# Performance work log

Measured on AMD Instinct MI355X. Metric: run time of the kernel, lower is better.

The kernel has to match this reference:

```python
import jax, jax.numpy as jnp
import numpy as np

B, S, D, H = 4, 2048, 1024, 16
HD = D // H  # head dim = 64


def setup_inputs() -> dict:
    key = jax.random.key(0)
    ks = jax.random.split(key, 11)
    std = 1.0 / np.sqrt(D)
    return {
        "query": jax.random.normal(ks[0], (B, S, D), jnp.float32),
        "key": jax.random.normal(ks[1], (B, S, D), jnp.float32),
        "value": jax.random.normal(ks[2], (B, S, D), jnp.float32),
        "Wq": jax.random.normal(ks[3], (D, D), jnp.float32) * std,
        "bq": jnp.zeros((D,), jnp.float32),
        "Wk": jax.random.normal(ks[4], (D, D), jnp.float32) * std,
        "bk": jnp.zeros((D,), jnp.float32),
        "Wv": jax.random.normal(ks[5], (D, D), jnp.float32) * std,
        "bv": jnp.zeros((D,), jnp.float32),
        "Wo": jax.random.normal(ks[6], (D, D), jnp.float32) * std,
        "bo": jnp.zeros((D,), jnp.float32),
    }


def reference(query, key, value, Wq, bq, Wk, bk, Wv, bv, Wo, bo):
    scale = jnp.sqrt(jnp.float32(D))  # NOTE: module scales by sqrt(hid_dim), not sqrt(head_dim)
    # nn.Linear: x @ W.T + b
    def split_heads(x):
        return x.reshape(B, -1, H, HD).transpose(0, 2, 1, 3)  # [B,H,S,HD]
    Q = split_heads(query @ Wq.T + bq)
    K = split_heads(key @ Wk.T + bk)
    V = split_heads(value @ Wv.T + bv)
    energy = jnp.einsum("bhqd,bhkd->bhqk", Q, K) / scale  # [B,H,S,S]
    attention = jax.nn.softmax(energy, axis=-1)  # dropout is identity in eval / p=0
    X = jnp.einsum("bhqk,bhkd->bhqd", attention, V)  # [B,H,S,HD]
    X = X.transpose(0, 2, 1, 3).reshape(B, -1, D)  # [B,S,D]
    return X @ Wo.T + bo
```

## Files before the change

### kernel.cpp

```cpp
#include <hip/hip_runtime.h>
#include <stdint.h>

#define DEVI __device__ __forceinline__

typedef __attribute__((ext_vector_type(8))) __bf16 bf16x8;
typedef __attribute__((ext_vector_type(4))) __bf16 bf16x4;
typedef __attribute__((ext_vector_type(4))) float f32x4;
typedef __attribute__((ext_vector_type(4))) unsigned short u16x4;
typedef __attribute__((ext_vector_type(4))) unsigned int u32x4;
typedef unsigned short u16;

constexpr int Bn = 4, Sn = 2048, Dn = 1024, Hn = 16;
constexpr int Mn = Bn * Sn;
constexpr float QSCALE = 1.4426950408889634f / 32.0f;
constexpr float SSHIFT = -16.0f;

DEVI u16 f2bf(float f) {
  uint32_t u = __builtin_bit_cast(uint32_t, f);
  u += 0x7fffu + ((u >> 16) & 1u);
  return (u16)(u >> 16);
}

typedef __attribute__((address_space(1))) void gvoid;
typedef __attribute__((address_space(3))) void lvoid;
DEVI void gload_lds16(const void* g, void* l) {
  __builtin_amdgcn_global_load_lds((gvoid*)(uintptr_t)g,
                                   (lvoid*)(uint32_t)(uintptr_t)l, 16, 0, 0);
}

DEVI f32x4 mfma16(bf16x8 a, bf16x8 b, f32x4 c) {
  return __builtin_amdgcn_mfma_f32_16x16x32_bf16(a, b, c, 0, 0, 0);
}

struct CastArgs {
  const float* src[7];
  u16* dst[7];
  int n[7];
};

__global__ __launch_bounds__(256) void cast_kernel(CastArgs a) {
  const int seg = blockIdx.y;
  const float* __restrict__ src = a.src[seg];
  u16* __restrict__ dst = a.dst[seg];
  const int n = a.n[seg];
  const int stride = gridDim.x * 256 * 4;
  for (int i = (blockIdx.x * 256 + threadIdx.x) * 4; i < n; i += stride) {
    const float4 v = *reinterpret_cast<const float4*>(src + i);
    u16x4 p;
    p[0] = f2bf(v.x); p[1] = f2bf(v.y); p[2] = f2bf(v.z); p[3] = f2bf(v.w);
    *reinterpret_cast<u16x4*>(dst + i) = p;
  }
}

struct QKVArgs {
  const u16 *Aq, *Ak, *Av, *Wq, *Wk, *Wv;
  const float *bq, *bk, *bv;
  u16 *Qh, *Kh, *Vt;
};

__global__ __launch_bounds__(256)
void qkv_gemm(QKVArgs a) {
  constexpr int BK = 32, Kd = 1024;
  __shared__ __align__(16) u16 As[128 * BK];
  __shared__ __align__(16) u16 Bs[128 * BK];

  const int raw = blockIdx.x;
  const int swz = (raw & 7) * 192 + (raw >> 3);
  const int which = swz >> 9;
  const int bid = swz & 511;
  const u16* __restrict__ A  = which == 0 ? a.Aq : which == 1 ? a.Ak : a.Av;
  const u16* __restrict__ Bt = which == 0 ? a.Wq : which == 1 ? a.Wk : a.Wv;
  const float* __restrict__ bias = which == 0 ? a.bq : which == 1 ? a.bk : a.bv;

  const int tid = threadIdx.x;
  const int lane = tid & 63;
  const int w = tid >> 6;
  const int wr = w >> 1, wc = w & 1;
  const int mt = bid >> 3, nt = bid & 7;
  const int m0 = mt * 128, n0 = nt * 128;
  const int c = lane & 15, g = lane >> 4;

  f32x4 acc[4][4] = {};

  const u16* aA[2];
  const u16* aB[2];
  int loff[2];
  #pragma unroll
  for (int i = 0; i < 2; ++i) {
    const int chunk = (i * 4 + w) * 64 + lane;
    const int row = chunk >> 2, col = (chunk & 3) * 8;
    aA[i] = A + (size_t)(m0 + row) * Kd + col;
    aB[i] = Bt + (size_t)(n0 + row) * Kd + col;
    loff[i] = (i * 4 + w) * 1024;
  }

  for (int kt = 0; kt < Kd; kt += BK) {
    #pragma unroll
    for (int i = 0; i < 2; ++i) {
      gload_lds16(aA[i] + kt, (char*)As + loff[i]);
      gload_lds16(aB[i] + kt, (char*)Bs + loff[i]);
    }
    __syncthreads();
    bf16x8 af[4], bfr[4];
    #pragma unroll
    for (int i = 0; i < 4; ++i) {
      af[i]  = *(const bf16x8*)(As + (wr * 64 + i * 16 + c) * BK + g * 8);
      bfr[i] = *(const bf16x8*)(Bs + (wc * 64 + i * 16 + c) * BK + g * 8);
    }
    #pragma unroll
    for (int mi = 0; mi < 4; ++mi)
      #pragma unroll
      for (int ni = 0; ni < 4; ++ni)
        acc[mi][ni] = mfma16(af[mi], bfr[ni], acc[mi][ni]);
    __syncthreads();
  }

  #pragma unroll
  for (int mi = 0; mi < 4; ++mi) {
    #pragma unroll
    for (int ni = 0; ni < 4; ++ni) {
      const int n = n0 + wc * 64 + ni * 16 + c;
      const float bv = bias[n];
      const int mb = m0 + wr * 64 + mi * 16 + g * 4;
      const f32x4 v = acc[mi][ni];
      const int h = n >> 6, hd = n & 63;
      if (which == 2) {
        const int b = mb >> 11, s = mb & 2047;
        u16x4 pk;
        #pragma unroll
        for (int j = 0; j < 4; ++j) pk[j] = f2bf(v[j] + bv);
        *(u16x4*)(a.Vt + ((size_t)((b * Hn + h) * 64 + hd)) * Sn + s) = pk;
      } else {
        u16* dst = which == 0 ? a.Qh : a.Kh;
        const float sc = which == 0 ? QSCALE : 1.0f;
        #pragma unroll
        for (int j = 0; j < 4; ++j) {
          const int m = mb + j;
          const int b = m >> 11, s = m & 2047;
          dst[(((size_t)(b * Hn + h) * Sn + s) << 6) + hd] = f2bf((v[j] + bv) * sc);
        }
      }
    }
  }
}

__global__ __launch_bounds__(256)
void gemm_out(const u16* __restrict__ A, const u16* __restrict__ Bt,
              const float* __restrict__ bias, float* __restrict__ out) {
  constexpr int BK = 32, Kd = 1024;
  __shared__ __align__(16) u16 As[128 * BK];
  __shared__ __align__(16) u16 Bs[128 * BK];

  const int raw = blockIdx.x;
  const int swz = (raw & 7) * 64 + (raw >> 3);
  const int tid = threadIdx.x;
  const int lane = tid & 63;
  const int w = tid >> 6;
  const int wr = w >> 1, wc = w & 1;
  const int mt = swz >> 3, nt = swz & 7;
  const int m0 = mt * 128, n0 = nt * 128;
  const int c = lane & 15, g = lane >> 4;

  f32x4 acc[4][4] = {};

  const u16* aA[2];
  const u16* aB[2];
  int loff[2];
  #pragma unroll
  for (int i = 0; i < 2; ++i) {
    const int chunk = (i * 4 + w) * 64 + lane;
    const int row = chunk >> 2, col = (chunk & 3) * 8;
    aA[i] = A + (size_t)(m0 + row) * Kd + col;
    aB[i] = Bt + (size_t)(n0 + row) * Kd + col;
    loff[i] = (i * 4 + w) * 1024;
  }

  for (int kt = 0; kt < Kd; kt += BK) {
    #pragma unroll
    for (int i = 0; i < 2; ++i) {
      gload_lds16(aA[i] + kt, (char*)As + loff[i]);
      gload_lds16(aB[i] + kt, (char*)Bs + loff[i]);
    }
    __syncthreads();
    bf16x8 af[4], bfr[4];
    #pragma unroll
    for (int i = 0; i < 4; ++i) {
      af[i]  = *(const bf16x8*)(As + (wr * 64 + i * 16 + c) * BK + g * 8);
      bfr[i] = *(const bf16x8*)(Bs + (wc * 64 + i * 16 + c) * BK + g * 8);
    }
    #pragma unroll
    for (int mi = 0; mi < 4; ++mi)
      #pragma unroll
      for (int ni = 0; ni < 4; ++ni)
        acc[mi][ni] = mfma16(af[mi], bfr[ni], acc[mi][ni]);
    __syncthreads();
  }

  #pragma unroll
  for (int mi = 0; mi < 4; ++mi) {
    #pragma unroll
    for (int ni = 0; ni < 4; ++ni) {
      const int n = n0 + wc * 64 + ni * 16 + c;
      const float bv = bias[n];
      const int mb = m0 + wr * 64 + mi * 16 + g * 4;
      const f32x4 v = acc[mi][ni];
      #pragma unroll
      for (int j = 0; j < 4; ++j)
        out[(size_t)(mb + j) * Dn + n] = v[j] + bv;
    }
  }
}

__global__ __launch_bounds__(512, 4)
void flash_attn(const u16* __restrict__ Q, const u16* __restrict__ K,
                const u16* __restrict__ Vt, u16* __restrict__ X) {
  __shared__ __align__(16) u16 Ks[3][4096];
  __shared__ __align__(16) u16 Vs[3][4096];

  const int tid = threadIdx.x, lane = tid & 63, w = tid >> 6;
  const int bid = blockIdx.x;
  const int bh = bid & 63, qt = bid >> 6;
  const int b = bh >> 4, h = bh & 15;
  const int q0 = qt * 128 + w * 16;
  const int c = lane & 15, g = lane >> 4;

  const u16* Qb = Q + (size_t)bh * Sn * 64;
  const u16* Kb = K + (size_t)bh * Sn * 64;
  const u16* Vb = Vt + (size_t)bh * 64 * Sn;

  const int srow = tid >> 3;
  const int scol = (((tid & 7) * 16) ^ ((srow & 7) << 4)) >> 1;
  const int srcK = srow * 64 + scol;
  const int srcV = srow * Sn + scol;
  const int ldsOff = w * 1024;
#define STAGE(BUF, KV_)                                                   \
  {                                                                       \
    gload_lds16(Kb + (size_t)(KV_) * 64 + srcK, (char*)Ks[BUF] + ldsOff); \
    gload_lds16(Vb + (KV_) + srcV, (char*)Vs[BUF] + ldsOff);              \
  }

  const int laneB0 = c * 128 + ((g * 16) ^ ((c & 7) << 4));
  const int laneB1 = c * 128 + ((64 + g * 16) ^ ((c & 7) << 4));

  bf16x8 qf[2];
  #pragma unroll
  for (int ks = 0; ks < 2; ++ks)
    qf[ks] = *(const bf16x8*)(Qb + (size_t)(q0 + c) * 64 + ks * 32 + g * 8);

  bf16x8 ONES;
  #pragma unroll
  for (int e = 0; e < 8; ++e) ONES[e] = (__bf16)1.0f;
  const f32x4 SINITv = {SSHIFT, SSHIFT, SSHIFT, SSHIFT};

  STAGE(0, 0);
  STAGE(1, 64);

  f32x4 o[4] = {};
  f32x4 lacc = {};

#define TILE(BUF, SBUF, KV)                                                   \
  {                                                                           \
    asm volatile("s_waitcnt vmcnt(2)" ::: "memory");                          \
    __builtin_amdgcn_sched_barrier(0);                                        \
    __builtin_amdgcn_s_barrier();                                             \
    __builtin_amdgcn_sched_barrier(0);                                        \
    STAGE(SBUF, ((KV) + 128) & (Sn - 1));                                     \
    f32x4 sc[4];                                                              \
    {                                                                         \
      bf16x8 kfr[4];                                                          \
      _Pragma("unroll")                                                       \
      for (int kf = 0; kf < 4; ++kf)                                          \
        kfr[kf] = *(const bf16x8*)((const char*)Ks[BUF] + laneB0 + kf * 2048);\
      __builtin_amdgcn_s_setprio(1);                                          \
      _Pragma("unroll")                                                       \
      for (int kf = 0; kf < 4; ++kf)                                          \
        sc[kf] = mfma16(kfr[kf], qf[0], SINITv);                              \
      __builtin_amdgcn_s_setprio(0);                                          \
      _Pragma("unroll")                                                       \
      for (int kf = 0; kf < 4; ++kf)                                          \
        kfr[kf] = *(const bf16x8*)((const char*)Ks[BUF] + laneB1 + kf * 2048);\
      __builtin_amdgcn_s_setprio(1);                                          \
      _Pragma("unroll")                                                       \
      for (int kf = 0; kf < 4; ++kf)                                          \
        sc[kf] = mfma16(kfr[kf], qf[1], sc[kf]);                              \
      __builtin_amdgcn_s_setprio(0);                                          \
    }                                                                         \
    uint32_t wvv[4][2];                                                       \
    _Pragma("unroll")                                                         \
    for (int kf = 0; kf < 4; ++kf) {                                          \
      const float p0 = __builtin_exp2f(sc[kf][0]);                            \
      const float p1 = __builtin_exp2f(sc[kf][1]);                            \
      const float p2 = __builtin_exp2f(sc[kf][2]);                            \
      const float p3 = __builtin_exp2f(sc[kf][3]);                            \
      asm("v_cvt_pk_bf16_f32 %0, %1, %2" : "=v"(wvv[kf][0]) : "v"(p0), "v"(p1)); \
      asm("v_cvt_pk_bf16_f32 %0, %1, %2" : "=v"(wvv[kf][1]) : "v"(p2), "v"(p3)); \
    }                                                                         \
    bf16x8 pa[2];                                                             \
    _Pragma("unroll")                                                         \
    for (int ks2 = 0; ks2 < 2; ++ks2) {                                       \
      uint32_t ua = wvv[2 * ks2][0], ub = wvv[2 * ks2][1];                    \
      uint32_t uc = wvv[2 * ks2 + 1][0], ud = wvv[2 * ks2 + 1][1];            \
      asm("v_permlane32_swap_b32 %0, %1" : "+v"(ua), "+v"(uc));               \
      asm("v_permlane32_swap_b32 %0, %1" : "+v"(ub), "+v"(ud));               \
      asm("v_permlane16_swap_b32 %0, %1" : "+v"(ua), "+v"(uc));               \
      asm("v_permlane16_swap_b32 %0, %1" : "+v"(ub), "+v"(ud));               \
      const u32x4 uv = {ua, ub, uc, ud};                                      \
      pa[ks2] = __builtin_bit_cast(bf16x8, uv);                               \
    }                                                                         \
    lacc = mfma16(pa[0], ONES, lacc);                                         \
    lacc = mfma16(pa[1], ONES, lacc);                                         \
    {                                                                         \
      bf16x8 vfr[4];                                                          \
      _Pragma("unroll")                                                       \
      for (int nd = 0; nd < 4; ++nd)                                          \
        vfr[nd] = *(const bf16x8*)((const char*)Vs[BUF] + laneB0 + nd * 2048);\
      __builtin_amdgcn_s_setprio(1);                                          \
      _Pragma("unroll")                                                       \
      for (int nd = 0; nd < 4; ++nd)                                          \
        o[nd] = mfma16(pa[0], vfr[nd], o[nd]);                                \
      __builtin_amdgcn_s_setprio(0);                                          \
      _Pragma("unroll")                                                       \
      for (int nd = 0; nd < 4; ++nd)                                          \
        vfr[nd] = *(const bf16x8*)((const char*)Vs[BUF] + laneB1 + nd * 2048);\
      __builtin_amdgcn_s_setprio(1);                                          \
      _Pragma("unroll")                                                       \
      for (int nd = 0; nd < 4; ++nd)                                          \
        o[nd] = mfma16(pa[1], vfr[nd], o[nd]);                                \
      __builtin_amdgcn_s_setprio(0);                                          \
    }                                                                         \
  }

  for (int kv = 0; kv < 1920; kv += 192) {
    TILE(0, 2, kv);
    TILE(1, 0, kv + 64);
    TILE(2, 1, kv + 128);
  }
  TILE(0, 2, 1920);
  TILE(1, 0, 1984);
#undef TILE
#undef STAGE

  #pragma unroll
  for (int j = 0; j < 4; ++j) {
    const float rn = 1.0f / lacc[j];
    const int s = q0 + g * 4 + j;
    u16* dst = X + (size_t)(b * Sn + s) * Dn + h * 64 + c;
    #pragma unroll
    for (int nd = 0; nd < 4; ++nd)
      dst[nd * 16] = f2bf(o[nd][j] * rn);
  }
}

extern "C" void kernel_launch(void* const* d_in, const int* in_sizes, int n_in,
                              void* d_out, int out_size, void* d_ws, size_t ws_size,
                              hipStream_t stream) {
  (void)in_sizes; (void)n_in; (void)out_size; (void)ws_size;
  const float* query = (const float*)d_in[0];
  const float* key_  = (const float*)d_in[1];
  const float* value = (const float*)d_in[2];
  const float* Wq = (const float*)d_in[3];
  const float* bq = (const float*)d_in[4];
  const float* Wk = (const float*)d_in[5];
  const float* bk = (const float*)d_in[6];
  const float* Wv = (const float*)d_in[7];
  const float* bv = (const float*)d_in[8];
  const float* Wo = (const float*)d_in[9];
  const float* bo = (const float*)d_in[10];

  char* ws = (char*)d_ws;
  size_t off = 0;
  auto alloc = [&](size_t bytes) {
    void* p = ws + off;
    off += (bytes + 255) & ~(size_t)255;
    return p;
  };
  const size_t actB = (size_t)Mn * Dn * 2;
  const size_t wB = (size_t)Dn * Dn * 2;
  u16* qbuf = (u16*)alloc(actB);
  u16* kbuf = (u16*)alloc(actB);
  u16* vbuf = (u16*)alloc(actB);
  u16* wqb = (u16*)alloc(wB);
  u16* wkb = (u16*)alloc(wB);
  u16* wvb = (u16*)alloc(wB);
  u16* wob = (u16*)alloc(wB);
  u16* Qh = (u16*)alloc(actB);
  u16* Kh = (u16*)alloc(actB);
  u16* Vt = (u16*)alloc(actB);
  u16* Xb = qbuf;

  CastArgs ca;
  ca.src[0] = query; ca.src[1] = key_; ca.src[2] = value;
  ca.src[3] = Wq; ca.src[4] = Wk; ca.src[5] = Wv; ca.src[6] = Wo;
  ca.dst[0] = qbuf; ca.dst[1] = kbuf; ca.dst[2] = vbuf;
  ca.dst[3] = wqb; ca.dst[4] = wkb; ca.dst[5] = wvb; ca.dst[6] = wob;
  ca.n[0] = ca.n[1] = ca.n[2] = Mn * Dn;
  ca.n[3] = ca.n[4] = ca.n[5] = ca.n[6] = Dn * Dn;
  cast_kernel<<<dim3(1024, 7), 256, 0, stream>>>(ca);

  QKVArgs qa;
  qa.Aq = qbuf; qa.Ak = kbuf; qa.Av = vbuf;
  qa.Wq = wqb; qa.Wk = wkb; qa.Wv = wvb;
  qa.bq = bq; qa.bk = bk; qa.bv = bv;
  qa.Qh = Qh; qa.Kh = Kh; qa.Vt = Vt;
  qkv_gemm<<<dim3(1536), 256, 0, stream>>>(qa);

  flash_attn<<<dim3(Bn * Hn * (Sn / 128)), 512, 0, stream>>>(Qh, Kh, Vt, Xb);
  gemm_out<<<dim3(512), 256, 0, stream>>>(Xb, wob, bo, (float*)d_out);
}
```

Baseline: 226.6 us.

## Triple-buffer GEMM K-loop with async LDS loads, swizzle, and 128x256 tiles

Both projection GEMMs move from 128x128 tiles on 256 threads, with one barrier pair per K step, to 128x256 tiles on 512 threads with a three-stage LDS ring. Global-to-LDS loads for the step two ahead are issued before the MFMAs of the current step, and a single barrier plus a partial vmcnt wait replaces the double sync. LDS addresses are XOR-swizzled to avoid bank conflicts, and MFMA sections run at raised wave priority. This is meant to hide memory latency and cut sync overhead, at the cost of more LDS per block, which may limit occupancy, and halved grid sizes.

```diff
diff --git a/kernel.cpp b/kernel.cpp
--- a/kernel.cpp
+++ b/kernel.cpp
@@ -52,68 +52,86 @@
   }
 }
 
+
+#define GEMM_PRE(Aptr, Btptr)                                                 \
+  const int tid = threadIdx.x, lane = tid & 63, w = tid >> 6;                 \
+  const int wr = w >> 2, wc = w & 3;                                          \
+  const int c = lane & 15, g = lane >> 4;                                     \
+  const int srow = tid >> 2;                                                  \
+  const int scolb = ((tid & 3) * 16) ^ ((srow & 3) << 4);                     \
+  const u16* aSrc  = (Aptr)  + (size_t)(m0 + srow) * 1024 + (scolb >> 1);     \
+  const u16* bSrc0 = (Btptr) + (size_t)(n0 + srow) * 1024 + (scolb >> 1);     \
+  const u16* bSrc1 = (Btptr) + (size_t)(n0 + 128 + srow) * 1024 + (scolb >> 1); \
+  const int ldsOff = w * 1024;                                                \
+  const int aB = (wr * 64 + c) * 64 + ((g * 16) ^ ((c & 3) << 4));            \
+  const int bB = (wc * 64 + c) * 64 + ((g * 16) ^ ((c & 3) << 4));
+
+#define GSTAGE(BUF, KT_)                                                      \
+  {                                                                           \
+    gload_lds16(aSrc + (KT_), (char*)As[BUF] + ldsOff);                       \
+    gload_lds16(bSrc0 + (KT_), (char*)Bs[BUF] + ldsOff);                      \
+    gload_lds16(bSrc1 + (KT_), (char*)Bs[BUF] + 8192 + ldsOff);               \
+  }
+
+#define GTILE(BUF, SBUF, KT)                                                  \
+  {                                                                           \
+    asm volatile("s_waitcnt vmcnt(3)" ::: "memory");                          \
+    __builtin_amdgcn_sched_barrier(0);                                        \
+    __builtin_amdgcn_s_barrier();                                             \
+    __builtin_amdgcn_sched_barrier(0);                                        \
+    GSTAGE(SBUF, ((KT) + 64) & 1023);                                         \
+    bf16x8 af[4], bfq[4];                                                     \
+    _Pragma("unroll")                                                         \
+    for (int i = 0; i < 4; ++i)                                               \
+      af[i] = *(const bf16x8*)((const char*)As[BUF] + aB + i * 1024);         \
+    _Pragma("unroll")                                                         \
+    for (int i = 0; i < 4; ++i)                                               \
+      bfq[i] = *(const bf16x8*)((const char*)Bs[BUF] + bB + i * 1024);        \
+    __builtin_amdgcn_s_setprio(1);                                            \
+    _Pragma("unroll")                                                         \
+    for (int mi = 0; mi < 4; ++mi)                                            \
+      _Pragma("unroll")                                                       \
+      for (int ni = 0; ni < 4; ++ni)                                          \
+        acc[mi][ni] = mfma16(af[mi], bfq[ni], acc[mi][ni]);                   \
+    __builtin_amdgcn_s_setprio(0);                                            \
+  }
+
+#define GEMM_LOOP                                                             \
+  GSTAGE(0, 0);                                                               \
+  GSTAGE(1, 32);                                                              \
+  for (int kt = 0; kt < 960; kt += 96) {                                      \
+    GTILE(0, 2, kt);                                                          \
+    GTILE(1, 0, kt + 32);                                                     \
+    GTILE(2, 1, kt + 64);                                                     \
+  }                                                                           \
+  GTILE(0, 2, 960);                                                           \
+  GTILE(1, 0, 992);
+
 struct QKVArgs {
   const u16 *Aq, *Ak, *Av, *Wq, *Wk, *Wv;
   const float *bq, *bk, *bv;
   u16 *Qh, *Kh, *Vt;
 };
 
-__global__ __launch_bounds__(256)
+__global__ __launch_bounds__(512, 4)
 void qkv_gemm(QKVArgs a) {
-  constexpr int BK = 32, Kd = 1024;
-  __shared__ __align__(16) u16 As[128 * BK];
-  __shared__ __align__(16) u16 Bs[128 * BK];
+  __shared__ __align__(16) u16 As[3][128 * 32];
+  __shared__ __align__(16) u16 Bs[3][256 * 32];
 
   const int raw = blockIdx.x;
-  const int swz = (raw & 7) * 192 + (raw >> 3);
-  const int which = swz >> 9;
-  const int bid = swz & 511;
+  const int swz = (raw & 7) * 96 + (raw >> 3);
+  const int which = swz >> 8;
+  const int bid = swz & 255;
   const u16* __restrict__ A  = which == 0 ? a.Aq : which == 1 ? a.Ak : a.Av;
   const u16* __restrict__ Bt = which == 0 ? a.Wq : which == 1 ? a.Wk : a.Wv;
   const float* __restrict__ bias = which == 0 ? a.bq : which == 1 ? a.bk : a.bv;
 
-  const int tid = threadIdx.x;
-  const int lane = tid & 63;
-  const int w = tid >> 6;
-  const int wr = w >> 1, wc = w & 1;
-  const int mt = bid >> 3, nt = bid & 7;
-  const int m0 = mt * 128, n0 = nt * 128;
-  const int c = lane & 15, g = lane >> 4;
-
+  const int mt = bid >> 2, nt = bid & 3;
+  const int m0 = mt * 128, n0 = nt * 256;
+
+  GEMM_PRE(A, Bt)
   f32x4 acc[4][4] = {};
-
-  const u16* aA[2];
-  const u16* aB[2];
-  int loff[2];
-  #pragma unroll
-  for (int i = 0; i < 2; ++i) {
-    const int chunk = (i * 4 + w) * 64 + lane;
-    const int row = chunk >> 2, col = (chunk & 3) * 8;
-    aA[i] = A + (size_t)(m0 + row) * Kd + col;
-    aB[i] = Bt + (size_t)(n0 + row) * Kd + col;
-    loff[i] = (i * 4 + w) * 1024;
-  }
-
-  for (int kt = 0; kt < Kd; kt += BK) {
-    #pragma unroll
-    for (int i = 0; i < 2; ++i) {
-      gload_lds16(aA[i] + kt, (char*)As + loff[i]);
-      gload_lds16(aB[i] + kt, (char*)Bs + loff[i]);
-    }
-    __syncthreads();
-    bf16x8 af[4], bfr[4];
-    #pragma unroll
-    for (int i = 0; i < 4; ++i) {
-      af[i]  = *(const bf16x8*)(As + (wr * 64 + i * 16 + c) * BK + g * 8);
-      bfr[i] = *(const bf16x8*)(Bs + (wc * 64 + i * 16 + c) * BK + g * 8);
-    }
-    #pragma unroll
-    for (int mi = 0; mi < 4; ++mi)
-      #pragma unroll
-      for (int ni = 0; ni < 4; ++ni)
-        acc[mi][ni] = mfma16(af[mi], bfr[ni], acc[mi][ni]);
-    __syncthreads();
-  }
+  GEMM_LOOP
 
   #pragma unroll
   for (int mi = 0; mi < 4; ++mi) {
@@ -144,57 +162,20 @@
   }
 }
 
-__global__ __launch_bounds__(256)
+__global__ __launch_bounds__(512, 4)
 void gemm_out(const u16* __restrict__ A, const u16* __restrict__ Bt,
               const float* __restrict__ bias, float* __restrict__ out) {
-  constexpr int BK = 32, Kd = 1024;
-  __shared__ __align__(16) u16 As[128 * BK];
-  __shared__ __align__(16) u16 Bs[128 * BK];
+  __shared__ __align__(16) u16 As[3][128 * 32];
+  __shared__ __align__(16) u16 Bs[3][256 * 32];
 
   const int raw = blockIdx.x;
-  const int swz = (raw & 7) * 64 + (raw >> 3);
-  const int tid = threadIdx.x;
-  const int lane = tid & 63;
-  const int w = tid >> 6;
-  const int wr = w >> 1, wc = w & 1;
-  const int mt = swz >> 3, nt = swz & 7;
-  const int m0 = mt * 128, n0 = nt * 128;
-  const int c = lane & 15, g = lane >> 4;
-
+  const int swz = (raw & 7) * 32 + (raw >> 3);
+  const int mt = swz >> 2, nt = swz & 3;
+  const int m0 = mt * 128, n0 = nt * 256;
+
+  GEMM_PRE(A, Bt)
   f32x4 acc[4][4] = {};
-
-  const u16* aA[2];
-  const u16* aB[2];
-  int loff[2];
-  #pragma unroll
-  for (int i = 0; i < 2; ++i) {
-    const int chunk = (i * 4 + w) * 64 + lane;
-    const int row = chunk >> 2, col = (chunk & 3) * 8;
-    aA[i] = A + (size_t)(m0 + row) * Kd + col;
-    aB[i] = Bt + (size_t)(n0 + row) * Kd + col;
-    loff[i] = (i * 4 + w) * 1024;
-  }
-
-  for (int kt = 0; kt < Kd; kt += BK) {
-    #pragma unroll
-    for (int i = 0; i < 2; ++i) {
-      gload_lds16(aA[i] + kt, (char*)As + loff[i]);
-      gload_lds16(aB[i] + kt, (char*)Bs + loff[i]);
-    }
-    __syncthreads();
-    bf16x8 af[4], bfr[4];
-    #pragma unroll
-    for (int i = 0; i < 4; ++i) {
-      af[i]  = *(const bf16x8*)(As + (wr * 64 + i * 16 + c) * BK + g * 8);
-      bfr[i] = *(const bf16x8*)(Bs + (wc * 64 + i * 16 + c) * BK + g * 8);
-    }
-    #pragma unroll
-    for (int mi = 0; mi < 4; ++mi)
-      #pragma unroll
-      for (int ni = 0; ni < 4; ++ni)
-        acc[mi][ni] = mfma16(af[mi], bfr[ni], acc[mi][ni]);
-    __syncthreads();
-  }
+  GEMM_LOOP
 
   #pragma unroll
   for (int mi = 0; mi < 4; ++mi) {
@@ -210,6 +191,11 @@
     }
   }
 }
+
+#undef GEMM_LOOP
+#undef GTILE
+#undef GSTAGE
+#undef GEMM_PRE
 
 __global__ __launch_bounds__(512, 4)
 void flash_attn(const u16* __restrict__ Q, const u16* __restrict__ K,
@@ -402,8 +388,8 @@
   qa.Wq = wqb; qa.Wk = wkb; qa.Wv = wvb;
   qa.bq = bq; qa.bk = bk; qa.bv = bv;
   qa.Qh = Qh; qa.Kh = Kh; qa.Vt = Vt;
-  qkv_gemm<<<dim3(1536), 256, 0, stream>>>(qa);
+  qkv_gemm<<<dim3(768), 512, 0, stream>>>(qa);
 
   flash_attn<<<dim3(Bn * Hn * (Sn / 128)), 512, 0, stream>>>(Qh, Kh, Vt, Xb);
-  gemm_out<<<dim3(512), 256, 0, stream>>>(Xb, wob, bo, (float*)d_out);
-}
+  gemm_out<<<dim3(256), 512, 0, stream>>>(Xb, wob, bo, (float*)d_out);
+}
```

Result: faster. 216.7 us (-4.4%).
